# Kernel tuning notes

Measured on AMD Instinct MI355X. Metric: run time of the kernel, lower is better.

## Reference

```python
import jax, jax.numpy as jnp
import numpy as np

B, N, P, D = 16, 1024, 72, 96
ND, H, K = 64, 4, 16
LN_EPS = 1e-5
ROW_EPS = 1e-8


def topk_sparsify(adj, k):
    # adj: (..., N, N); keep top-k per row (scatter-mask), then row-renormalize
    shp = adj.shape
    n = shp[-1]
    flat = adj.reshape(-1, n)
    _, idx = jax.lax.top_k(flat, k)  # (R, k)
    rows = jnp.arange(flat.shape[0])[:, None]
    mask = jnp.zeros_like(flat).at[rows, idx].set(1.0)
    sp = flat * mask
    sp = sp / (sp.sum(-1, keepdims=True) + ROW_EPS)
    return sp.reshape(shp)


def setup_inputs() -> dict:
    key = jax.random.key(0)
    ks = jax.random.split(key, 12)
    xav1 = np.sqrt(6.0 / (N + ND))  # xavier_uniform bound for (N, ND)
    inp = {
        "patch_features": jax.random.normal(ks[0], (B, N, P, D), jnp.float32),
        "E1": jax.random.uniform(ks[1], (H, N, ND), jnp.float32, -xav1, xav1),
        "E2": jax.random.uniform(ks[2], (H, ND, N), jnp.float32, -xav1, xav1),
        "temperature": jnp.full((H,), 0.5, jnp.float32),
        "fusion_weight": jnp.float32(0.5),
        "dW1": jax.random.normal(ks[3], (D, ND), jnp.float32) / np.sqrt(D),
        "db1": jnp.zeros((ND,), jnp.float32),
        "ln_g": jnp.ones((ND,), jnp.float32),
        "ln_b": jnp.zeros((ND,), jnp.float32),
        "dW2": jax.random.normal(ks[4], (ND, ND), jnp.float32) / np.sqrt(ND),
        "db2": jnp.zeros((ND,), jnp.float32),
        "eW1": jax.random.normal(ks[5], (H, 2 * H), jnp.float32) / np.sqrt(H),
        "eb1": jnp.zeros((2 * H,), jnp.float32),
        "eW2": jax.random.normal(ks[6], (2 * H, 1), jnp.float32) / np.sqrt(2 * H),
        "eb2": jnp.zeros((1,), jnp.float32),
    }
    return inp


def reference(patch_features, E1, E2, temperature, fusion_weight,
              dW1, db1, ln_g, ln_b, dW2, db2, eW1, eb1, eW2, eb2):
    # ---- static multi-head graphs: softmax(relu(E1 @ E2) / T, axis=-1) ----
    s = jax.nn.relu(jnp.einsum('hnd,hdm->hnm', E1, E2))
    static_adjs = jax.nn.softmax(s / temperature[:, None, None], axis=-1)

    # ---- dynamic graphs from mean-pooled patch features ----
    node_repr = patch_features.mean(axis=2)                 # (B, N, D)
    h1 = node_repr @ dW1 + db1                              # (B, N, ND)
    mu = h1.mean(-1, keepdims=True)
    var = ((h1 - mu) ** 2).mean(-1, keepdims=True)
    h1 = (h1 - mu) / jnp.sqrt(var + LN_EPS) * ln_g + ln_b   # LayerNorm
    h1 = jax.nn.relu(h1)                                    # (dropout = identity, eval)
    dyn_emb = h1 @ dW2 + db2                                # (B, N, ND)
    d = jax.nn.relu(jnp.einsum('bnd,hdm->bhnm', dyn_emb, E2))
    dynamic_adjs = jax.nn.softmax(d / temperature[None, :, None, None], axis=-1)

    # ---- top-k sparsify + row renormalize ----
    static_adjs = topk_sparsify(static_adjs, K)             # (H, N, N)
    dynamic_adjs = topk_sparsify(dynamic_adjs, K)           # (B, H, N, N)

    # ---- fuse static + dynamic ----
    fused = (1.0 - fusion_weight) * static_adjs[None] + fusion_weight * dynamic_adjs

    # ---- edge MLP over head dim: (B, N, N, H) -> (B, N, N) ----
    x = jnp.transpose(fused, (0, 2, 3, 1))                  # (B, N, N, H)
    ew = jax.nn.relu(x @ eW1 + eb1) @ eW2 + eb2             # (B, N, N, 1)
    final_adjs = jax.nn.sigmoid(ew[..., 0]) * fused.mean(axis=1)
    return final_adjs, static_adjs, dynamic_adjs
```

## Files before the change

### kernel.cpp

```cpp
#include <hip/hip_runtime.h>

typedef unsigned int u32;
typedef unsigned long long u64;

#define Bn 16
#define Nn 1024
#define Pp 72
#define MARG 3e-4f

#define NEGINF __int_as_float(0xff800000)
#define POSINF __int_as_float(0x7f800000)

#define DPP_STEP(OP, CTRL, RM)                                                 \
  y = __builtin_amdgcn_update_dpp(__float_as_int(v), __float_as_int(v),        \
                                  CTRL, RM, 0xf, false);                       \
  v = OP(v, __int_as_float(y));

#define DPP_RED(NAME, OP)                                                      \
  __device__ __forceinline__ float NAME(float v) {                             \
    int y;                                                                     \
    DPP_STEP(OP, 0x111, 0xf)                                                   \
    DPP_STEP(OP, 0x112, 0xf)                                                   \
    DPP_STEP(OP, 0x114, 0xf)                                                   \
    DPP_STEP(OP, 0x118, 0xf)                                                   \
    DPP_STEP(OP, 0x142, 0xa)                                                   \
    DPP_STEP(OP, 0x143, 0xc)                                                   \
    return __int_as_float(__builtin_amdgcn_readlane(__float_as_int(v), 63));   \
  }

#define FADDOP(a, b) ((a) + (b))
DPP_RED(dmaxf, fmaxf)
DPP_RED(dminf, fminf)
DPP_RED(dsumf, FADDOP)

__device__ __forceinline__ u32 wminu(u32 v) {
#pragma unroll
  for (int off = 1; off < 64; off <<= 1) {
    u32 o = (u32)__shfl_xor((int)v, off, 64);
    v = (o < v) ? o : v;
  }
  return v;
}

template <int MODE>
__device__ __forceinline__ u32 select_row(const float* __restrict__ q,
                                          float* __restrict__ v, int l,
                                          const float* __restrict__ e1row,
                                          const double* __restrict__ edrow,
                                          const float* __restrict__ e2t,
                                          double Td) {
  float lm = q[0];
#pragma unroll
  for (int j = 1; j < 16; ++j) lm = fmaxf(lm, q[j]);
  const float qmax = dmaxf(lm);

  u32 lo = 0u, hi = __float_as_uint(qmax) + 1u;
  u32 kept = 0u;
  bool f16 = false;
  float pvf = 0.0f;
#pragma unroll 1
  while (hi - lo > 1u) {
    u32 mid = (lo + hi) >> 1;
    float pv = __uint_as_float(mid);
    u32 cw = 0;
#pragma unroll
    for (int j = 0; j < 16; ++j)
      cw += (u32)__popcll(__ballot(q[j] >= pv));
    if (cw >= 16u) lo = mid; else hi = mid;
    if (cw == 16u) { f16 = true; pvf = pv; break; }
  }
  float theta, ub;
  if (f16) {
    float vmin = POSINF, umax = -1.0f;
#pragma unroll
    for (int j = 0; j < 16; ++j) {
      if (q[j] >= pvf) { kept |= 1u << j; vmin = fminf(vmin, q[j]); }
      else umax = fmaxf(umax, q[j]);
    }
    theta = dminf(vmin);
    ub = dmaxf(umax);
  } else {
    theta = __uint_as_float(lo);
    u32 cw = 0;
#pragma unroll
    for (int j = 0; j < 16; ++j) {
      cw += (u32)__popcll(__ballot(q[j] > theta));
      if (q[j] > theta) kept |= 1u << j;
    }
    int rr = 16 - (int)cw;
#pragma unroll 1
    for (int it = 0; it < rr; ++it) {
      u32 mc = 0xFFFFFFFFu;
#pragma unroll
      for (int j = 0; j < 16; ++j)
        if (q[j] == theta && !((kept >> j) & 1u)) {
          u32 cc = (u32)((j << 6) | l);
          mc = cc < mc ? cc : mc;
        }
      u32 wm = wminu(mc);
      if ((wm & 63u) == (u32)l) kept |= 1u << (wm >> 6);
    }
    ub = theta;
  }

  if (theta - ub >= MARG) {
    float e[16];
    float es = 0.0f, ek = 0.0f;
#pragma unroll
    for (int j = 0; j < 16; ++j) {
      e[j] = __expf(q[j] - qmax);
      es += e[j];
      if ((kept >> j) & 1u) ek += e[j];
    }
    const float Z = dsumf(es);
    const float EK = dsumf(ek);
    const float inv = 1.0f / (EK + 1e-8f * Z);
#pragma unroll
    for (int j = 0; j < 16; ++j)
      v[j] = ((kept >> j) & 1u) ? (e[j] * inv) : 0.0f;
    return kept;
  } else {
    double qd[16];
    const float thr = ub - MARG;
#pragma unroll 1
    for (int j = 0; j < 16; ++j) {
      if (q[j] >= thr) {
        const int m = l + (j << 6);
        const float* col = e2t + (size_t)m * 64;
        double a = 0.0;
        for (int d = 0; d < 64; ++d) {
          double s = (MODE == 0) ? (double)e1row[d] : edrow[d];
          a = fma(s, (double)col[d], a);
        }
        qd[j] = (a > 0.0 ? a : 0.0) / Td;
      } else {
        qd[j] = (double)q[j];
      }
    }
    double bm = qd[0];
#pragma unroll
    for (int j = 1; j < 16; ++j) bm = qd[j] > bm ? qd[j] : bm;
    float mh = (float)bm;
    float mlo = (float)(bm - (double)mh);
    float whi = dmaxf(mh);
    float wlo = dmaxf(mh == whi ? mlo : NEGINF);
    const double qmaxd = (double)whi + (double)wlo;

    float ev2[16];
    float es2 = 0.0f;
#pragma unroll
    for (int j = 0; j < 16; ++j) { ev2[j] = __expf((float)(qd[j] - qmaxd)); es2 += ev2[j]; }
    const float Z2 = dsumf(es2);

    u32 kept2 = 0;
    float EK2 = 0.0f;
#pragma unroll 1
    for (int it = 0; it < 16; ++it) {
      double bv = -1.0;
      int bjj = -1;
#pragma unroll
      for (int j = 0; j < 16; ++j) {
        bool tk = (((kept2 >> j) & 1u) == 0u) && (qd[j] > bv);
        bv = tk ? qd[j] : bv;
        bjj = tk ? j : bjj;
      }
      float bh = NEGINF, bl = NEGINF;
      if (bjj >= 0) { bh = (float)bv; bl = (float)(bv - (double)bh); }
      float vhi = dmaxf(bh);
      float vlo = dmaxf(bh == vhi ? bl : NEGINF);
      bool elig = (bh == vhi) && (bl == vlo);
      u32 mc = elig ? (u32)((bjj << 6) | l) : 0xFFFFFFFFu;
      u32 mwin = wminu(mc);
      EK2 += __expf((float)(((double)vhi + (double)vlo) - qmaxd));
      if ((mwin & 63u) == (u32)l) kept2 |= 1u << (mwin >> 6);
    }
    const float inv2 = 1.0f / (EK2 + 1e-8f * Z2);
#pragma unroll
    for (int j = 0; j < 16; ++j)
      v[j] = ((kept2 >> j) & 1u) ? (ev2[j] * inv2) : 0.0f;
    return kept2;
  }
}

__device__ __forceinline__ void emit_compact(u32 kept, const float* __restrict__ v,
                                             int l, float* __restrict__ cbase) {
  const u64 lt = ((u64)1 << l) - 1;
  u32 cum = 0;
#pragma unroll
  for (int j = 0; j < 16; ++j) {
    u64 m = __ballot((kept >> j) & 1u);
    u32 idx = cum + (u32)__popcll(m & lt);
    if ((kept >> j) & 1u) {
      cbase[idx] = v[j];
      cbase[16 + idx] = __uint_as_float((u32)(l + (j << 6)));
    }
    cum += (u32)__popcll(m);
  }
}

__global__ __launch_bounds__(256) void k_e2t(const float* __restrict__ E2,
                                             float* __restrict__ E2T) {
  __shared__ float tile[32][65];
  const int h = blockIdx.x >> 5;
  const int m0 = (blockIdx.x & 31) << 5;
  const float* src = E2 + (size_t)h * 65536;
  float* dst = E2T + (size_t)h * 65536;
  const int t = threadIdx.x;
#pragma unroll
  for (int k = 0; k < 8; ++k) {
    int idx = k * 256 + t;
    int d = idx >> 5, mm = idx & 31;
    tile[mm][d] = src[d * 1024 + m0 + mm];
  }
  __syncthreads();
#pragma unroll
  for (int k = 0; k < 8; ++k) {
    int idx = k * 256 + t;
    int mm = idx >> 6, d = idx & 63;
    dst[(size_t)(m0 + mm) * 64 + d] = tile[mm][d];
  }
}

__global__ __launch_bounds__(128) void k_meanmlp(const float* __restrict__ pf,
                                                 const float* __restrict__ dW1,
                                                 const float* __restrict__ db1,
                                                 const float* __restrict__ ln_g,
                                                 const float* __restrict__ ln_b,
                                                 const float* __restrict__ dW2,
                                                 const float* __restrict__ db2,
                                                 double* __restrict__ embD,
                                                 float* __restrict__ embF) {
  __shared__ double ndD[96];
  __shared__ double red[64];
  __shared__ double h1r[64];
  const int t = threadIdx.x;
  const int bn = blockIdx.x;

  if (t < 96) {
    const float* src = pf + (size_t)bn * (Pp * 96) + t;
    double s = 0.0;
    for (int p = 0; p < Pp; ++p) s += (double)src[p * 96];
    ndD[t] = s / 72.0;
  }
  __syncthreads();

  double a = 0.0;
  if (t < 64) {
    a = (double)db1[t];
    for (int d = 0; d < 96; ++d) a = fma(ndD[d], (double)dW1[d * 64 + t], a);
    red[t] = a;
  }
  __syncthreads();
  for (int s2 = 32; s2 >= 1; s2 >>= 1) {
    if (t < s2) red[t] += red[t + s2];
    __syncthreads();
  }
  const double mu = red[0] * (1.0 / 64.0);
  __syncthreads();
  const double dv = a - mu;
  if (t < 64) red[t] = dv * dv;
  __syncthreads();
  for (int s2 = 32; s2 >= 1; s2 >>= 1) {
    if (t < s2) red[t] += red[t + s2];
    __syncthreads();
  }
  const double var = red[0] * (1.0 / 64.0);
  if (t < 64) {
    double xn = dv / sqrt(var + 1e-5) * (double)ln_g[t] + (double)ln_b[t];
    h1r[t] = xn > 0.0 ? xn : 0.0;
  }
  __syncthreads();
  if (t < 64) {
    double e = (double)db2[t];
    for (int k = 0; k < 64; ++k) e = fma(h1r[k], (double)dW2[k * 64 + t], e);
    embD[(size_t)bn * 64 + t] = e;
    embF[(size_t)bn * 64 + t] = (float)e;
  }
}

template <int MODE>
__global__ __launch_bounds__(256) void k_dotsel(const float* __restrict__ e1f,
                                                const float* __restrict__ embF,
                                                const double* __restrict__ embD,
                                                const float* __restrict__ E2,
                                                const float* __restrict__ E2T,
                                                const float* __restrict__ temp,
                                                float* __restrict__ outp,
                                                float* __restrict__ cmp) {
  __shared__ float embsh[64][8];
  __shared__ float lgs[4][1024];
  const int t = threadIdx.x;
  const int r0 = blockIdx.x * 8;
  int h;
  size_t erow;
  if (MODE == 0) {
    h = r0 >> 10;
    erow = (size_t)r0;
  } else {
    int b = r0 >> 12;
    h = (r0 >> 10) & 3;
    int n0 = r0 & 1023;
    erow = (size_t)(b << 10) + n0;
  }
  const float* efa = (MODE == 0) ? (e1f + erow * 64) : (embF + erow * 64);
  const float* e2 = E2 + (size_t)h * 65536;
  const float* e2t = E2T + (size_t)h * 65536;
  const float invT = 1.0f / temp[h];
  const double Td = (double)temp[h];

  for (int i = t; i < 512; i += 256) {
    int g = i & 7, d = i >> 3;
    embsh[d][g] = efa[g * 64 + d];
  }
  __syncthreads();

  const int s = t >> 7;
  const int c1 = (t & 127) * 4;
  const int c2 = c1 + 512;

  float acc[4][8];
#pragma unroll
  for (int g = 0; g < 4; ++g)
#pragma unroll
    for (int x = 0; x < 8; ++x) acc[g][x] = 0.0f;

#pragma unroll 4
  for (int d = 0; d < 64; ++d) {
    float4 va = *(const float4*)(e2 + d * 1024 + c1);
    float4 vb = *(const float4*)(e2 + d * 1024 + c2);
    float4 ea = *(const float4*)&embsh[d][4 * s];
    float sg;
#define ROWFMA(g, SS)                                                          \
    sg = SS;                                                                   \
    acc[g][0] = fmaf(sg, va.x, acc[g][0]);                                     \
    acc[g][1] = fmaf(sg, va.y, acc[g][1]);                                     \
    acc[g][2] = fmaf(sg, va.z, acc[g][2]);                                     \
    acc[g][3] = fmaf(sg, va.w, acc[g][3]);                                     \
    acc[g][4] = fmaf(sg, vb.x, acc[g][4]);                                     \
    acc[g][5] = fmaf(sg, vb.y, acc[g][5]);                                     \
    acc[g][6] = fmaf(sg, vb.z, acc[g][6]);                                     \
    acc[g][7] = fmaf(sg, vb.w, acc[g][7]);
    ROWFMA(0, ea.x) ROWFMA(1, ea.y) ROWFMA(2, ea.z) ROWFMA(3, ea.w)
#undef ROWFMA
  }
#pragma unroll
  for (int g = 0; g < 4; ++g)
#pragma unroll
    for (int x = 0; x < 8; ++x) acc[g][x] = fmaxf(acc[g][x], 0.0f) * invT;

  const int w = t >> 6, l = t & 63;

#pragma unroll
  for (int gr = 0; gr < 2; ++gr) {
    if (s == gr) {
#pragma unroll
      for (int k = 0; k < 4; ++k) {
        float4 o1, o2;
        o1.x = acc[k][0]; o1.y = acc[k][1]; o1.z = acc[k][2]; o1.w = acc[k][3];
        o2.x = acc[k][4]; o2.y = acc[k][5]; o2.z = acc[k][6]; o2.w = acc[k][7];
        *(float4*)&lgs[k][c1] = o1;
        *(float4*)&lgs[k][c2] = o2;
      }
    }
    __syncthreads();
    {
      const int rloc = gr * 4 + w;
      const size_t r = (size_t)r0 + rloc;
      float q[16], v[16];
#pragma unroll
      for (int j = 0; j < 16; ++j) q[j] = lgs[w][l + (j << 6)];
      u32 kept = select_row<MODE>(
          q, v, l, (MODE == 0) ? (e1f + r * 64) : nullptr,
          (MODE == 1) ? (embD + (erow + rloc) * 64) : nullptr, e2t, Td);
      float* row = outp + r * 1024;
#pragma unroll
      for (int j = 0; j < 16; ++j) row[l + (j << 6)] = v[j];
      emit_compact(kept, v, l, cmp + r * 32);
    }
    __syncthreads();
  }
}

__global__ __launch_bounds__(256) void k_fusec(const float* __restrict__ cmpd,
                                               const float* __restrict__ cmp0,
                                               float* __restrict__ fin,
                                               const float* __restrict__ eW1,
                                               const float* __restrict__ eb1,
                                               const float* __restrict__ eW2,
                                               const float* __restrict__ eb2,
                                               const float* __restrict__ fwp) {
  __shared__ float fused[4][1024];
  const int t = threadIdx.x;
  const int bn = blockIdx.x;
  const int b = bn >> 10, n = bn & 1023;
  const float fw = fwp[0];
  const float w1 = 1.0f - fw;

  float4* fz = (float4*)&fused[0][0];
  float4 z; z.x = 0.f; z.y = 0.f; z.z = 0.f; z.w = 0.f;
#pragma unroll
  for (int k = 0; k < 4; ++k) fz[t + 256 * k] = z;
  __syncthreads();

  if (t < 64) {
    int h = t >> 4, k = t & 15;
    const float* cb = cmp0 + ((size_t)(h * 1024 + n)) * 32;
    float val = cb[k];
    int col = (int)__float_as_uint(cb[16 + k]);
    fused[h][col] = w1 * val;
  }
  __syncthreads();
  if (t < 64) {
    int h = t >> 4, k = t & 15;
    const float* cb = cmpd + ((size_t)((b * 4 + h) * 1024 + n)) * 32;
    float val = cb[k];
    int col = (int)__float_as_uint(cb[16 + k]);
    fused[h][col] += fw * val;
  }
  __syncthreads();

  float W1[4][8], B1v[8], W2v[8];
#pragma unroll
  for (int hh = 0; hh < 4; ++hh)
#pragma unroll
    for (int j = 0; j < 8; ++j) W1[hh][j] = eW1[hh * 8 + j];
#pragma unroll
  for (int j = 0; j < 8; ++j) { B1v[j] = eb1[j]; W2v[j] = eW2[j]; }
  const float b2 = eb2[0];

  float* orow = fin + (size_t)bn * 1024;
#pragma unroll
  for (int k = 0; k < 4; ++k) {
    const int col = t + 256 * k;
    const float f0 = fused[0][col];
    const float f1 = fused[1][col];
    const float f2 = fused[2][col];
    const float f3 = fused[3][col];
    float ew = b2;
#pragma unroll
    for (int j = 0; j < 8; ++j) {
      float hj = B1v[j];
      hj = fmaf(f0, W1[0][j], hj);
      hj = fmaf(f1, W1[1][j], hj);
      hj = fmaf(f2, W1[2][j], hj);
      hj = fmaf(f3, W1[3][j], hj);
      ew = fmaf(fmaxf(hj, 0.0f), W2v[j], ew);
    }
    const float mean = (f0 + f1 + f2 + f3) * 0.25f;
    const float sg = 1.0f / (1.0f + __expf(-ew));
    orow[col] = sg * mean;
  }
}

extern "C" void kernel_launch(void* const* d_in, const int* in_sizes, int n_in,
                              void* d_out, int out_size, void* d_ws, size_t ws_size,
                              hipStream_t stream) {
  const float* pf   = (const float*)d_in[0];
  const float* E1   = (const float*)d_in[1];
  const float* E2   = (const float*)d_in[2];
  const float* temp = (const float*)d_in[3];
  const float* fw   = (const float*)d_in[4];
  const float* dW1  = (const float*)d_in[5];
  const float* db1  = (const float*)d_in[6];
  const float* ln_g = (const float*)d_in[7];
  const float* ln_b = (const float*)d_in[8];
  const float* dW2  = (const float*)d_in[9];
  const float* db2  = (const float*)d_in[10];
  const float* eW1  = (const float*)d_in[11];
  const float* eb1  = (const float*)d_in[12];
  const float* eW2  = (const float*)d_in[13];
  const float* eb2  = (const float*)d_in[14];

  float* out_final = (float*)d_out;
  float* out_stat  = out_final + (size_t)Bn * Nn * Nn;
  float* out_dyn   = out_stat + (size_t)4 * Nn * Nn;

  char* wsb = (char*)d_ws;
  double* embD = (double*)wsb;
  float* embF  = (float*)(wsb + (8u << 20));
  float* E2T   = (float*)(wsb + (12u << 20));
  float* cmp0  = (float*)(wsb + (13u << 20));
  float* cmpd  = (float*)(wsb + (14u << 20));

  k_e2t<<<128, 256, 0, stream>>>(E2, E2T);
  k_meanmlp<<<Bn * Nn, 128, 0, stream>>>(pf, dW1, db1, ln_g, ln_b, dW2, db2, embD, embF);
  k_dotsel<0><<<512, 256, 0, stream>>>(E1, nullptr, nullptr, E2, E2T, temp, out_stat, cmp0);
  k_dotsel<1><<<8192, 256, 0, stream>>>(nullptr, embF, embD, E2, E2T, temp, out_dyn, cmpd);
  k_fusec<<<16384, 256, 0, stream>>>(cmpd, cmp0, out_final, eW1, eb1, eW2, eb2, fw);
}
```

Measured before the change: 609.0 us.

## Split fused dot-select kernel into separate logits and top-k selection kernels

Separates the per-row dot-product/logit computation from the top-k selection into two kernels. The dot kernel now handles 16 rows per block with an 8x8 register tile and writes relu-scaled logits directly to the output buffer. A new selection kernel reads them back one row per wavefront, without shared-memory staging or block syncs. This improves register-tile reuse and decouples occupancy of the two phases, but adds a full global-memory round trip of the logit tensor.

New measurement: 574.4 us. 1.06x faster.

```diff
diff --git a/kernel.cpp b/kernel.cpp
--- a/kernel.cpp
+++ b/kernel.cpp
@@ -279,18 +279,14 @@
 }
 
 template <int MODE>
-__global__ __launch_bounds__(256) void k_dotsel(const float* __restrict__ e1f,
-                                                const float* __restrict__ embF,
-                                                const double* __restrict__ embD,
-                                                const float* __restrict__ E2,
-                                                const float* __restrict__ E2T,
-                                                const float* __restrict__ temp,
-                                                float* __restrict__ outp,
-                                                float* __restrict__ cmp) {
-  __shared__ float embsh[64][8];
-  __shared__ float lgs[4][1024];
+__global__ __launch_bounds__(256) void k_dot(const float* __restrict__ e1f,
+                                             const float* __restrict__ embF,
+                                             const float* __restrict__ E2,
+                                             const float* __restrict__ temp,
+                                             float* __restrict__ outp) {
+  __shared__ float embsh[64][16];
   const int t = threadIdx.x;
-  const int r0 = blockIdx.x * 8;
+  const int r0 = blockIdx.x * 16;
   int h;
   size_t erow;
   if (MODE == 0) {
@@ -304,12 +300,11 @@
   }
   const float* efa = (MODE == 0) ? (e1f + erow * 64) : (embF + erow * 64);
   const float* e2 = E2 + (size_t)h * 65536;
-  const float* e2t = E2T + (size_t)h * 65536;
   const float invT = 1.0f / temp[h];
-  const double Td = (double)temp[h];
-
-  for (int i = t; i < 512; i += 256) {
-    int g = i & 7, d = i >> 3;
+
+#pragma unroll
+  for (int i = t; i < 1024; i += 256) {
+    int g = i & 15, d = i >> 4;
     embsh[d][g] = efa[g * 64 + d];
   }
   __syncthreads();
@@ -318,9 +313,9 @@
   const int c1 = (t & 127) * 4;
   const int c2 = c1 + 512;
 
-  float acc[4][8];
-#pragma unroll
-  for (int g = 0; g < 4; ++g)
+  float acc[8][8];
+#pragma unroll
+  for (int g = 0; g < 8; ++g)
 #pragma unroll
     for (int x = 0; x < 8; ++x) acc[g][x] = 0.0f;
 
@@ -328,7 +323,8 @@
   for (int d = 0; d < 64; ++d) {
     float4 va = *(const float4*)(e2 + d * 1024 + c1);
     float4 vb = *(const float4*)(e2 + d * 1024 + c2);
-    float4 ea = *(const float4*)&embsh[d][4 * s];
+    float4 ea = *(const float4*)&embsh[d][8 * s];
+    float4 eb = *(const float4*)&embsh[d][8 * s + 4];
     float sg;
 #define ROWFMA(g, SS)                                                          \
     sg = SS;                                                                   \
@@ -341,44 +337,63 @@
     acc[g][6] = fmaf(sg, vb.z, acc[g][6]);                                     \
     acc[g][7] = fmaf(sg, vb.w, acc[g][7]);
     ROWFMA(0, ea.x) ROWFMA(1, ea.y) ROWFMA(2, ea.z) ROWFMA(3, ea.w)
+    ROWFMA(4, eb.x) ROWFMA(5, eb.y) ROWFMA(6, eb.z) ROWFMA(7, eb.w)
 #undef ROWFMA
   }
-#pragma unroll
-  for (int g = 0; g < 4; ++g)
-#pragma unroll
-    for (int x = 0; x < 8; ++x) acc[g][x] = fmaxf(acc[g][x], 0.0f) * invT;
-
+
+#pragma unroll
+  for (int g = 0; g < 8; ++g) {
+    float* orow = outp + (size_t)(r0 + 8 * s + g) * 1024;
+    float4 o1, o2;
+    o1.x = fmaxf(acc[g][0], 0.0f) * invT;
+    o1.y = fmaxf(acc[g][1], 0.0f) * invT;
+    o1.z = fmaxf(acc[g][2], 0.0f) * invT;
+    o1.w = fmaxf(acc[g][3], 0.0f) * invT;
+    o2.x = fmaxf(acc[g][4], 0.0f) * invT;
+    o2.y = fmaxf(acc[g][5], 0.0f) * invT;
+    o2.z = fmaxf(acc[g][6], 0.0f) * invT;
+    o2.w = fmaxf(acc[g][7], 0.0f) * invT;
+    *(float4*)(orow + c1) = o1;
+    *(float4*)(orow + c2) = o2;
+  }
+}
+
+template <int MODE>
+__global__ __launch_bounds__(256) void k_selc(const float* __restrict__ e1f,
+                                              const double* __restrict__ embD,
+                                              const float* __restrict__ E2T,
+                                              const float* __restrict__ temp,
+                                              float* __restrict__ outp,
+                                              float* __restrict__ cmp) {
+  const int t = threadIdx.x;
   const int w = t >> 6, l = t & 63;
-
-#pragma unroll
-  for (int gr = 0; gr < 2; ++gr) {
-    if (s == gr) {
-#pragma unroll
-      for (int k = 0; k < 4; ++k) {
-        float4 o1, o2;
-        o1.x = acc[k][0]; o1.y = acc[k][1]; o1.z = acc[k][2]; o1.w = acc[k][3];
-        o2.x = acc[k][4]; o2.y = acc[k][5]; o2.z = acc[k][6]; o2.w = acc[k][7];
-        *(float4*)&lgs[k][c1] = o1;
-        *(float4*)&lgs[k][c2] = o2;
-      }
-    }
-    __syncthreads();
-    {
-      const int rloc = gr * 4 + w;
-      const size_t r = (size_t)r0 + rloc;
-      float q[16], v[16];
-#pragma unroll
-      for (int j = 0; j < 16; ++j) q[j] = lgs[w][l + (j << 6)];
-      u32 kept = select_row<MODE>(
-          q, v, l, (MODE == 0) ? (e1f + r * 64) : nullptr,
-          (MODE == 1) ? (embD + (erow + rloc) * 64) : nullptr, e2t, Td);
-      float* row = outp + r * 1024;
-#pragma unroll
-      for (int j = 0; j < 16; ++j) row[l + (j << 6)] = v[j];
-      emit_compact(kept, v, l, cmp + r * 32);
-    }
-    __syncthreads();
-  }
+  const int r = blockIdx.x * 4 + w;
+  int h;
+  size_t erow;
+  if (MODE == 0) {
+    h = r >> 10;
+    erow = (size_t)r;
+  } else {
+    int b = r >> 12;
+    h = (r >> 10) & 3;
+    int n = r & 1023;
+    erow = (size_t)(b << 10) + n;
+  }
+  const float* e2t = E2T + (size_t)h * 65536;
+  const double Td = (double)temp[h];
+  float* row = outp + (size_t)r * 1024;
+
+  float q[16], v[16];
+#pragma unroll
+  for (int j = 0; j < 16; ++j) q[j] = row[l + (j << 6)];
+
+  u32 kept = select_row<MODE>(q, v, l,
+                              (MODE == 0) ? (e1f + erow * 64) : nullptr,
+                              (MODE == 1) ? (embD + erow * 64) : nullptr,
+                              e2t, Td);
+#pragma unroll
+  for (int j = 0; j < 16; ++j) row[l + (j << 6)] = v[j];
+  emit_compact(kept, v, l, cmp + (size_t)r * 32);
 }
 
 __global__ __launch_bounds__(256) void k_fusec(const float* __restrict__ cmpd,
@@ -484,7 +499,9 @@
 
   k_e2t<<<128, 256, 0, stream>>>(E2, E2T);
   k_meanmlp<<<Bn * Nn, 128, 0, stream>>>(pf, dW1, db1, ln_g, ln_b, dW2, db2, embD, embF);
-  k_dotsel<0><<<512, 256, 0, stream>>>(E1, nullptr, nullptr, E2, E2T, temp, out_stat, cmp0);
-  k_dotsel<1><<<8192, 256, 0, stream>>>(nullptr, embF, embD, E2, E2T, temp, out_dyn, cmpd);
+  k_dot<0><<<256, 256, 0, stream>>>(E1, nullptr, E2, temp, out_stat);
+  k_selc<0><<<1024, 256, 0, stream>>>(E1, nullptr, E2T, temp, out_stat, cmp0);
+  k_dot<1><<<4096, 256, 0, stream>>>(nullptr, embF, E2, temp, out_dyn);
+  k_selc<1><<<16384, 256, 0, stream>>>(nullptr, embD, E2T, temp, out_dyn, cmpd);
   k_fusec<<<16384, 256, 0, stream>>>(cmpd, cmp0, out_final, eW1, eb1, eW2, eb2, fw);
 }
```
